# Kernel optimization log

Hardware: AMD Instinct MI355X
Metric: run time of the kernel (lower is better)

## Reference

```python
import jax, jax.numpy as jnp
import numpy as np

T, N = 12, 1000          # frames, pedestrians
RNN, EMB, GS, OUT = 128, 64, 4, 5
G = GS * GS              # 16 grid cells


def lstm_cell(x, h, c, W_ih, W_hh, b_ih, b_hh):
    # PyTorch LSTMCell gate order: i, f, g, o
    gates = x @ W_ih.T + h @ W_hh.T + b_ih + b_hh
    i, f, g, o = jnp.split(gates, 4, axis=-1)
    c_new = jax.nn.sigmoid(f) * c + jax.nn.sigmoid(i) * jnp.tanh(g)
    h_new = jax.nn.sigmoid(o) * jnp.tanh(c_new)
    return h_new, c_new


def setup_inputs() -> dict:
    key = jax.random.key(0)
    ks = jax.random.split(key, 10)
    s = 0.02  # small init scale for weights
    # binary occupancy grid masks: grid[f, n, p, g] = 1 if ped p falls in cell g of ped n's neighborhood
    grids = (jax.random.uniform(ks[1], (T, N, N, G)) < 0.02).astype(jnp.float32)
    return {
        "input_data": jax.random.normal(ks[0], (T, N, 2), dtype=jnp.float32),
        "grids": grids,
        "hidden_states": jnp.zeros((N, RNN), dtype=jnp.float32),
        "cell_states": jnp.zeros((N, RNN), dtype=jnp.float32),
        "W_in": jax.random.normal(ks[2], (EMB, 2)) * s,
        "b_in": jnp.zeros((EMB,), dtype=jnp.float32),
        "W_soc": jax.random.normal(ks[3], (EMB, G * RNN)) * s,
        "b_soc": jnp.zeros((EMB,), dtype=jnp.float32),
        "W_ih": jax.random.normal(ks[4], (4 * RNN, 2 * EMB)) * s,
        "W_hh": jax.random.normal(ks[5], (4 * RNN, RNN)) * s,
        "b_ih": jnp.zeros((4 * RNN,), dtype=jnp.float32),
        "b_hh": jnp.zeros((4 * RNN,), dtype=jnp.float32),
        "W_out": jax.random.normal(ks[6], (OUT, RNN)) * s,
        "b_out": jnp.zeros((OUT,), dtype=jnp.float32),
    }


def reference(input_data, grids, hidden_states, cell_states,
              W_in, b_in, W_soc, b_soc, W_ih, W_hh, b_ih, b_hh, W_out, b_out):
    def step(carry, frame):
        h, c = carry
        x, grid = frame  # x: [N,2], grid: [N,N,G]
        # social pooling: for each node n, grid[n].T @ h  -> [G, RNN]
        social = jnp.einsum('npg,ph->ngh', grid, h).reshape(N, G * RNN)
        ie = jax.nn.relu(x @ W_in.T + b_in)           # [N, EMB]
        te = jax.nn.relu(social @ W_soc.T + b_soc)    # [N, EMB]
        emb = jnp.concatenate([ie, te], axis=-1)      # [N, 2*EMB]
        h, c = lstm_cell(emb, h, c, W_ih, W_hh, b_ih, b_hh)
        out = h @ W_out.T + b_out                     # [N, OUT]
        return (h, c), out

    (h, c), outputs = jax.lax.scan(step, (hidden_states, cell_states),
                                   (input_data, grids))
    return outputs, h, c  # outputs: [T, N, OUT]
```

## Files before the change

kernel.cpp:

```cpp
#include <hip/hip_runtime.h>
#include <hip/hip_bf16.h>


#define TT   12
#define NN   1000
#define RNNW 128
#define EMBW 64
#define GGW  16
#define OUTD 5
#define UCW  (GGW*EMBW)
#define AKW  256
#define NGATE 512
#define GROW (NN*GGW)

__device__ __forceinline__ float sigmf(float x) { return 1.f / (1.f + __expf(-x)); }

__global__ void k_init(const float* __restrict__ h0, const float* __restrict__ c0,
                       float* __restrict__ h, float* __restrict__ c) {
    int i = blockIdx.x * 256 + threadIdx.x;
    if (i < NN * RNNW) { h[i] = h0[i]; c[i] = c0[i]; }
}

__global__ __launch_bounds__(256) void k_U(const float* __restrict__ h,
                                           const float* __restrict__ Wsoc,
                                           float* __restrict__ U) {
    __shared__ float sA[32][RNNW];
    __shared__ float sB[64][RNNW + 1];
    const int tid = threadIdx.x;
    const int p0 = blockIdx.x * 32;
    const int g  = blockIdx.y;
    {
        int r = tid >> 3, c0_ = (tid & 7) * 16;
        int p = p0 + r;
        const float4 z = {0.f, 0.f, 0.f, 0.f};
        #pragma unroll
        for (int q = 0; q < 4; q++) {
            float4 v = z;
            if (p < NN) v = *(const float4*)(h + (size_t)p * RNNW + c0_ + q * 4);
            *(float4*)(&sA[r][c0_ + q * 4]) = v;
        }
    }
    {
        int e = tid >> 2, c0_ = (tid & 3) * 32;
        const float* src = Wsoc + (size_t)e * (GGW * RNNW) + g * RNNW + c0_;
        #pragma unroll
        for (int q = 0; q < 8; q++) {
            float4 v = *(const float4*)(src + q * 4);
            sB[e][c0_ + q * 4 + 0] = v.x;
            sB[e][c0_ + q * 4 + 1] = v.y;
            sB[e][c0_ + q * 4 + 2] = v.z;
            sB[e][c0_ + q * 4 + 3] = v.w;
        }
    }
    __syncthreads();
    const int tx = tid & 63, ty = tid >> 6;
    float acc[8];
    #pragma unroll
    for (int i = 0; i < 8; i++) acc[i] = 0.f;
    for (int k = 0; k < RNNW; k++) {
        float b = sB[tx][k];
        #pragma unroll
        for (int i = 0; i < 8; i++) acc[i] += sA[ty + 4 * i][k] * b;
    }
    #pragma unroll
    for (int i = 0; i < 8; i++) {
        int p = p0 + ty + 4 * i;
        if (p < NN) U[(size_t)p * UCW + g * EMBW + tx] = acc[i];
    }
}

__global__ __launch_bounds__(512) void k_pool(const unsigned int* __restrict__ grids,
                                              const float* __restrict__ x_in,
                                              const float* __restrict__ U,
                                              const float* __restrict__ h,
                                              const float* __restrict__ W_in,
                                              const float* __restrict__ b_in,
                                              const float* __restrict__ b_soc,
                                              float* __restrict__ A, int t) {
    const int n = blockIdx.x;
    const int tid = threadIdx.x;
    const int lane = tid & 63, wave = tid >> 6;
    const unsigned int* gp = grids + ((size_t)t * NN + n) * (size_t)GROW;
    float acc = 0.f;
    for (int it = 0; it < 8; ++it) {
        int base = (it * 8 + wave) * 256;
        if (base >= GROW) break;
        int f0 = base + lane * 4;
        uint4 v = {0u, 0u, 0u, 0u};
        if (f0 < GROW) v = *(const uint4*)(gp + f0);
        unsigned int va[4] = {v.x, v.y, v.z, v.w};
        #pragma unroll
        for (int sub = 0; sub < 4; ++sub) {
            unsigned long long m = __ballot(va[sub] != 0u);
            while (m) {
                int b = __builtin_ctzll(m); m &= m - 1;
                int f = base + b * 4 + sub;
                int p = f >> 4, g = f & 15;
                acc += U[(size_t)p * UCW + g * EMBW + lane];
            }
        }
    }
    __shared__ float sAcc[8][64];
    sAcc[wave][lane] = acc;
    __syncthreads();
    if (tid < 64) {
        float s = 0.f;
        #pragma unroll
        for (int w = 0; w < 8; w++) s += sAcc[w][tid];
        float te = fmaxf(s + b_soc[tid], 0.f);
        float x0 = x_in[((size_t)t * NN + n) * 2 + 0];
        float x1 = x_in[((size_t)t * NN + n) * 2 + 1];
        float ie = fmaxf(W_in[tid * 2 + 0] * x0 + W_in[tid * 2 + 1] * x1 + b_in[tid], 0.f);
        A[(size_t)n * AKW + tid] = ie;
        A[(size_t)n * AKW + EMBW + tid] = te;
    } else if (tid >= 128 && tid < 256) {
        int k = tid - 128;
        A[(size_t)n * AKW + 128 + k] = h[(size_t)n * RNNW + k];
    }
}

__global__ __launch_bounds__(256) void k_gates(const float* __restrict__ A,
                                               const float* __restrict__ W_ih,
                                               const float* __restrict__ W_hh,
                                               const float* __restrict__ b_ih,
                                               const float* __restrict__ b_hh,
                                               float* __restrict__ gates) {
    __shared__ float sA[32][128];
    __shared__ float sB[64][129];
    const int tid = threadIdx.x;
    const int n0 = blockIdx.x * 32;
    const int j0 = blockIdx.y * 64;
    const int tx = tid & 63, ty = tid >> 6;
    float acc[8];
    #pragma unroll
    for (int i = 0; i < 8; i++) acc[i] = 0.f;
    for (int kk = 0; kk < 2; ++kk) {
        __syncthreads();
        {
            int r = tid >> 3, c0_ = (tid & 7) * 16;
            int n = n0 + r;
            const float4 z = {0.f, 0.f, 0.f, 0.f};
            #pragma unroll
            for (int q = 0; q < 4; q++) {
                float4 v = z;
                if (n < NN) v = *(const float4*)(A + (size_t)n * AKW + kk * 128 + c0_ + q * 4);
                *(float4*)(&sA[r][c0_ + q * 4]) = v;
            }
        }
        {
            int e = tid >> 2, c0_ = (tid & 3) * 32;
            const float* W = kk ? W_hh : W_ih;
            const float* src = W + (size_t)(j0 + e) * 128 + c0_;
            #pragma unroll
            for (int q = 0; q < 8; q++) {
                float4 v = *(const float4*)(src + q * 4);
                sB[e][c0_ + q * 4 + 0] = v.x;
                sB[e][c0_ + q * 4 + 1] = v.y;
                sB[e][c0_ + q * 4 + 2] = v.z;
                sB[e][c0_ + q * 4 + 3] = v.w;
            }
        }
        __syncthreads();
        for (int k = 0; k < 128; k++) {
            float b = sB[tx][k];
            #pragma unroll
            for (int i = 0; i < 8; i++) acc[i] += sA[ty + 4 * i][k] * b;
        }
    }
    float bias = b_ih[j0 + tx] + b_hh[j0 + tx];
    #pragma unroll
    for (int i = 0; i < 8; i++) {
        int n = n0 + ty + 4 * i;
        if (n < NN) gates[(size_t)n * NGATE + j0 + tx] = acc[i] + bias;
    }
}

__global__ __launch_bounds__(256) void k_lstm(const float* __restrict__ gates,
                                              float* __restrict__ h, float* __restrict__ c,
                                              const float* __restrict__ W_out,
                                              const float* __restrict__ b_out,
                                              float* __restrict__ out, int t) {
    __shared__ float sh[2][128];
    int tid = threadIdx.x;
    int local = tid >> 7;
    int r = tid & 127;
    int n = blockIdx.x * 2 + local;
    float hn = 0.f;
    if (n < NN) {
        const float* gr = gates + (size_t)n * NGATE;
        float gi = gr[r], gf = gr[128 + r], gg = gr[256 + r], go = gr[384 + r];
        float cn = sigmf(gf) * c[(size_t)n * RNNW + r] + sigmf(gi) * tanhf(gg);
        hn = sigmf(go) * tanhf(cn);
        c[(size_t)n * RNNW + r] = cn;
        h[(size_t)n * RNNW + r] = hn;
    }
    sh[local][r] = hn;
    __syncthreads();
    if (n < NN && r < OUTD) {
        float s = b_out[r];
        const float* wr = W_out + r * RNNW;
        for (int k = 0; k < RNNW; k++) s += sh[local][k] * wr[k];
        out[((size_t)t * NN + n) * OUTD + r] = s;
    }
}

__global__ void k_final(const float* __restrict__ h, const float* __restrict__ c,
                        float* __restrict__ out) {
    int i = blockIdx.x * 256 + threadIdx.x;
    if (i < NN * RNNW) {
        out[TT * NN * OUTD + i] = h[i];
        out[TT * NN * OUTD + NN * RNNW + i] = c[i];
    }
}

extern "C" void kernel_launch(void* const* d_in, const int* in_sizes, int n_in,
                              void* d_out, int out_size, void* d_ws, size_t ws_size,
                              hipStream_t stream) {
    const float* x_in        = (const float*)d_in[0];
    const unsigned int* grd  = (const unsigned int*)d_in[1];
    const float* h0          = (const float*)d_in[2];
    const float* c0          = (const float*)d_in[3];
    const float* W_in        = (const float*)d_in[4];
    const float* b_in        = (const float*)d_in[5];
    const float* W_soc       = (const float*)d_in[6];
    const float* b_soc       = (const float*)d_in[7];
    const float* W_ih        = (const float*)d_in[8];
    const float* W_hh        = (const float*)d_in[9];
    const float* b_ih        = (const float*)d_in[10];
    const float* b_hh        = (const float*)d_in[11];
    const float* W_out       = (const float*)d_in[12];
    const float* b_out       = (const float*)d_in[13];
    float* out = (float*)d_out;

    float* h     = (float*)d_ws;
    float* c     = h + NN * RNNW;
    float* U     = c + NN * RNNW;
    float* A     = U + (size_t)NN * UCW;
    float* gates = A + (size_t)NN * AKW;

    hipLaunchKernelGGL(k_init, dim3(500), dim3(256), 0, stream, h0, c0, h, c);
    for (int t = 0; t < TT; ++t) {
        hipLaunchKernelGGL(k_U,     dim3(32, 16), dim3(256), 0, stream, h, W_soc, U);
        hipLaunchKernelGGL(k_pool,  dim3(NN),     dim3(512), 0, stream, grd, x_in, U, h, W_in, b_in, b_soc, A, t);
        hipLaunchKernelGGL(k_gates, dim3(32, 8),  dim3(256), 0, stream, A, W_ih, W_hh, b_ih, b_hh, gates);
        hipLaunchKernelGGL(k_lstm,  dim3(500),    dim3(256), 0, stream, gates, h, c, W_out, b_out, out, t);
    }
    hipLaunchKernelGGL(k_final, dim3(500), dim3(256), 0, stream, h, c, out);
}
```

Baseline: 734.0 us.

## Pre-transpose weights and use register-blocked outer-product tiles in U and gate GEMMs

```diff
diff --git a/kernel.cpp b/kernel.cpp
--- a/kernel.cpp
+++ b/kernel.cpp
@@ -15,57 +15,84 @@
 
 __device__ __forceinline__ float sigmf(float x) { return 1.f / (1.f + __expf(-x)); }
 
-__global__ void k_init(const float* __restrict__ h0, const float* __restrict__ c0,
-                       float* __restrict__ h, float* __restrict__ c) {
+__global__ void k_prep(const float* __restrict__ h0, const float* __restrict__ c0,
+                       const float* __restrict__ W_soc,
+                       const float* __restrict__ W_ih, const float* __restrict__ W_hh,
+                       float* __restrict__ h, float* __restrict__ c,
+                       float* __restrict__ WsT, float* __restrict__ WcT) {
     int i = blockIdx.x * 256 + threadIdx.x;
-    if (i < NN * RNNW) { h[i] = h0[i]; c[i] = c0[i]; }
+    if (i < 131072) {
+        int e = i >> 11, gk = i & 2047;
+        WsT[gk * 64 + e] = W_soc[i];
+    } else if (i < 196608) {
+        int i2 = i - 131072;
+        int j = i2 >> 7, k = i2 & 127;
+        WcT[k * 512 + j] = W_ih[i2];
+    } else if (i < 262144) {
+        int i3 = i - 196608;
+        int j = i3 >> 7, k = i3 & 127;
+        WcT[(128 + k) * 512 + j] = W_hh[i3];
+    } else if (i < 262144 + NN * RNNW) {
+        int i4 = i - 262144; h[i4] = h0[i4];
+    } else if (i < 262144 + 2 * NN * RNNW) {
+        int i5 = i - 262144 - NN * RNNW; c[i5] = c0[i5];
+    }
 }
 
 __global__ __launch_bounds__(256) void k_U(const float* __restrict__ h,
-                                           const float* __restrict__ Wsoc,
+                                           const float* __restrict__ WsT,
                                            float* __restrict__ U) {
-    __shared__ float sA[32][RNNW];
-    __shared__ float sB[64][RNNW + 1];
+    __shared__ float sAT[RNNW][64];
+    __shared__ float sBT[RNNW][64];
     const int tid = threadIdx.x;
-    const int p0 = blockIdx.x * 32;
+    const int p0 = blockIdx.x * 64;
     const int g  = blockIdx.y;
     {
-        int r = tid >> 3, c0_ = (tid & 7) * 16;
-        int p = p0 + r;
-        const float4 z = {0.f, 0.f, 0.f, 0.f};
-        #pragma unroll
-        for (int q = 0; q < 4; q++) {
-            float4 v = z;
-            if (p < NN) v = *(const float4*)(h + (size_t)p * RNNW + c0_ + q * 4);
-            *(float4*)(&sA[r][c0_ + q * 4]) = v;
+        int pp = tid >> 2, kq = (tid & 3) * 4;
+        int p = p0 + pp;
+        #pragma unroll
+        for (int pass = 0; pass < 8; ++pass) {
+            int k0 = pass * 16 + kq;
+            float4 v = {0.f, 0.f, 0.f, 0.f};
+            if (p < NN) v = *(const float4*)(h + (size_t)p * RNNW + k0);
+            sAT[k0 + 0][pp] = v.x; sAT[k0 + 1][pp] = v.y;
+            sAT[k0 + 2][pp] = v.z; sAT[k0 + 3][pp] = v.w;
         }
     }
     {
-        int e = tid >> 2, c0_ = (tid & 3) * 32;
-        const float* src = Wsoc + (size_t)e * (GGW * RNNW) + g * RNNW + c0_;
-        #pragma unroll
-        for (int q = 0; q < 8; q++) {
-            float4 v = *(const float4*)(src + q * 4);
-            sB[e][c0_ + q * 4 + 0] = v.x;
-            sB[e][c0_ + q * 4 + 1] = v.y;
-            sB[e][c0_ + q * 4 + 2] = v.z;
-            sB[e][c0_ + q * 4 + 3] = v.w;
+        #pragma unroll
+        for (int pass = 0; pass < 8; ++pass) {
+            int f = pass * 256 + tid;
+            int k = f >> 4, e4 = (f & 15) * 4;
+            float4 v = *(const float4*)(WsT + (size_t)(g * 128 + k) * 64 + e4);
+            *(float4*)(&sBT[k][e4]) = v;
         }
     }
     __syncthreads();
-    const int tx = tid & 63, ty = tid >> 6;
-    float acc[8];
-    #pragma unroll
-    for (int i = 0; i < 8; i++) acc[i] = 0.f;
-    for (int k = 0; k < RNNW; k++) {
-        float b = sB[tx][k];
-        #pragma unroll
-        for (int i = 0; i < 8; i++) acc[i] += sA[ty + 4 * i][k] * b;
-    }
-    #pragma unroll
-    for (int i = 0; i < 8; i++) {
-        int p = p0 + ty + 4 * i;
-        if (p < NN) U[(size_t)p * UCW + g * EMBW + tx] = acc[i];
+    const int tx = tid & 15, ty = tid >> 4;
+    float acc[4][4];
+    #pragma unroll
+    for (int i = 0; i < 4; i++)
+        #pragma unroll
+        for (int j = 0; j < 4; j++) acc[i][j] = 0.f;
+    #pragma unroll 4
+    for (int k = 0; k < RNNW; ++k) {
+        float4 a4 = *(const float4*)(&sAT[k][ty * 4]);
+        float4 b4 = *(const float4*)(&sBT[k][tx * 4]);
+        const float av[4] = {a4.x, a4.y, a4.z, a4.w};
+        const float bv[4] = {b4.x, b4.y, b4.z, b4.w};
+        #pragma unroll
+        for (int i = 0; i < 4; i++)
+            #pragma unroll
+            for (int j = 0; j < 4; j++) acc[i][j] += av[i] * bv[j];
+    }
+    #pragma unroll
+    for (int i = 0; i < 4; i++) {
+        int p = p0 + ty * 4 + i;
+        if (p < NN) {
+            float4 v = {acc[i][0], acc[i][1], acc[i][2], acc[i][3]};
+            *(float4*)(U + (size_t)p * UCW + g * EMBW + tx * 4) = v;
+        }
     }
 }
 
@@ -120,58 +147,68 @@
 }
 
 __global__ __launch_bounds__(256) void k_gates(const float* __restrict__ A,
-                                               const float* __restrict__ W_ih,
-                                               const float* __restrict__ W_hh,
+                                               const float* __restrict__ WcT,
                                                const float* __restrict__ b_ih,
                                                const float* __restrict__ b_hh,
                                                float* __restrict__ gates) {
-    __shared__ float sA[32][128];
-    __shared__ float sB[64][129];
+    __shared__ float sAT[128][32];
+    __shared__ float sBT[128][64];
     const int tid = threadIdx.x;
     const int n0 = blockIdx.x * 32;
     const int j0 = blockIdx.y * 64;
-    const int tx = tid & 63, ty = tid >> 6;
-    float acc[8];
-    #pragma unroll
-    for (int i = 0; i < 8; i++) acc[i] = 0.f;
-    for (int kk = 0; kk < 2; ++kk) {
+    const int tx = tid & 15, ty = tid >> 4;
+    float acc[2][4];
+    #pragma unroll
+    for (int i = 0; i < 2; i++)
+        #pragma unroll
+        for (int j = 0; j < 4; j++) acc[i][j] = 0.f;
+    for (int kc = 0; kc < 2; ++kc) {
         __syncthreads();
         {
-            int r = tid >> 3, c0_ = (tid & 7) * 16;
-            int n = n0 + r;
-            const float4 z = {0.f, 0.f, 0.f, 0.f};
-            #pragma unroll
-            for (int q = 0; q < 4; q++) {
-                float4 v = z;
-                if (n < NN) v = *(const float4*)(A + (size_t)n * AKW + kk * 128 + c0_ + q * 4);
-                *(float4*)(&sA[r][c0_ + q * 4]) = v;
+            int nn = tid >> 3, kq = (tid & 7) * 4;
+            int n = n0 + nn;
+            #pragma unroll
+            for (int pass = 0; pass < 4; ++pass) {
+                int k0 = pass * 32 + kq;
+                float4 v = {0.f, 0.f, 0.f, 0.f};
+                if (n < NN) v = *(const float4*)(A + (size_t)n * AKW + kc * 128 + k0);
+                sAT[k0 + 0][nn] = v.x; sAT[k0 + 1][nn] = v.y;
+                sAT[k0 + 2][nn] = v.z; sAT[k0 + 3][nn] = v.w;
             }
         }
         {
-            int e = tid >> 2, c0_ = (tid & 3) * 32;
-            const float* W = kk ? W_hh : W_ih;
-            const float* src = W + (size_t)(j0 + e) * 128 + c0_;
-            #pragma unroll
-            for (int q = 0; q < 8; q++) {
-                float4 v = *(const float4*)(src + q * 4);
-                sB[e][c0_ + q * 4 + 0] = v.x;
-                sB[e][c0_ + q * 4 + 1] = v.y;
-                sB[e][c0_ + q * 4 + 2] = v.z;
-                sB[e][c0_ + q * 4 + 3] = v.w;
+            #pragma unroll
+            for (int pass = 0; pass < 8; ++pass) {
+                int f = pass * 256 + tid;
+                int k = f >> 4, e4 = (f & 15) * 4;
+                float4 v = *(const float4*)(WcT + (size_t)(kc * 128 + k) * NGATE + j0 + e4);
+                *(float4*)(&sBT[k][e4]) = v;
             }
         }
         __syncthreads();
-        for (int k = 0; k < 128; k++) {
-            float b = sB[tx][k];
-            #pragma unroll
-            for (int i = 0; i < 8; i++) acc[i] += sA[ty + 4 * i][k] * b;
-        }
-    }
-    float bias = b_ih[j0 + tx] + b_hh[j0 + tx];
-    #pragma unroll
-    for (int i = 0; i < 8; i++) {
-        int n = n0 + ty + 4 * i;
-        if (n < NN) gates[(size_t)n * NGATE + j0 + tx] = acc[i] + bias;
+        #pragma unroll 4
+        for (int k = 0; k < 128; ++k) {
+            float2 a2 = *(const float2*)(&sAT[k][ty * 2]);
+            float4 b4 = *(const float4*)(&sBT[k][tx * 4]);
+            const float av[2] = {a2.x, a2.y};
+            const float bv[4] = {b4.x, b4.y, b4.z, b4.w};
+            #pragma unroll
+            for (int i = 0; i < 2; i++)
+                #pragma unroll
+                for (int j = 0; j < 4; j++) acc[i][j] += av[i] * bv[j];
+        }
+    }
+    float4 bi = *(const float4*)(b_ih + j0 + tx * 4);
+    float4 bh = *(const float4*)(b_hh + j0 + tx * 4);
+    float bias[4] = {bi.x + bh.x, bi.y + bh.y, bi.z + bh.z, bi.w + bh.w};
+    #pragma unroll
+    for (int i = 0; i < 2; i++) {
+        int n = n0 + ty * 2 + i;
+        if (n < NN) {
+            float4 v = {acc[i][0] + bias[0], acc[i][1] + bias[1],
+                        acc[i][2] + bias[2], acc[i][3] + bias[3]};
+            *(float4*)(gates + (size_t)n * NGATE + j0 + tx * 4) = v;
+        }
     }
 }
 
@@ -237,12 +274,15 @@
     float* U     = c + NN * RNNW;
     float* A     = U + (size_t)NN * UCW;
     float* gates = A + (size_t)NN * AKW;
-
-    hipLaunchKernelGGL(k_init, dim3(500), dim3(256), 0, stream, h0, c0, h, c);
+    float* WsT   = gates + (size_t)NN * NGATE;
+    float* WcT   = WsT + 2048 * 64;
+
+    hipLaunchKernelGGL(k_prep, dim3(2024), dim3(256), 0, stream,
+                       h0, c0, W_soc, W_ih, W_hh, h, c, WsT, WcT);
     for (int t = 0; t < TT; ++t) {
-        hipLaunchKernelGGL(k_U,     dim3(32, 16), dim3(256), 0, stream, h, W_soc, U);
+        hipLaunchKernelGGL(k_U,     dim3(16, 16), dim3(256), 0, stream, h, WsT, U);
         hipLaunchKernelGGL(k_pool,  dim3(NN),     dim3(512), 0, stream, grd, x_in, U, h, W_in, b_in, b_soc, A, t);
-        hipLaunchKernelGGL(k_gates, dim3(32, 8),  dim3(256), 0, stream, A, W_ih, W_hh, b_ih, b_hh, gates);
+        hipLaunchKernelGGL(k_gates, dim3(32, 8),  dim3(256), 0, stream, A, WcT, b_ih, b_hh, gates);
         hipLaunchKernelGGL(k_lstm,  dim3(500),    dim3(256), 0, stream, gates, h, c, W_out, b_out, out, t);
     }
     hipLaunchKernelGGL(k_final, dim3(500), dim3(256), 0, stream, h, c, out);
```

Measured after the change: 664.2 us. 1.11x faster.
